# Optimization experiments

Measured on AMD Instinct MI355X. Metric: run time of the kernel, lower is better.

## Reference

```python
import jax, jax.numpy as jnp
import numpy as np

WS = 16          # window_size
OWS = 24         # overlap_win_size = int(ws*0.5) + ws
PAD = (OWS - WS) // 2
NH = 6           # num_heads


def _ln(x, g, b):
    m = jnp.mean(x, axis=-1, keepdims=True)
    v = jnp.mean((x - m) ** 2, axis=-1, keepdims=True)
    return (x - m) * jax.lax.rsqrt(v + 1e-5) * g + b


def setup_inputs() -> dict:
    key = jax.random.key(0)
    ks = jax.random.split(key, 12)
    B, H, W, C = 4, 64, 64, 180
    std = 0.02
    x = jax.random.normal(ks[0], (B, H * W, C), jnp.float32)
    y = jax.random.normal(ks[1], (B, H * W, C), jnp.float32)
    kv_w = jax.random.normal(ks[2], (2 * C, C), jnp.float32) * std
    kv_b = jnp.zeros((2 * C,), jnp.float32)
    q_w = jax.random.normal(ks[3], (C, C), jnp.float32) * std
    q_b = jnp.zeros((C,), jnp.float32)
    rpb = jax.random.normal(ks[4], ((WS + OWS - 1) ** 2, NH), jnp.float32) * std
    proj_w = jax.random.normal(ks[5], (C, C), jnp.float32) * std
    proj_b = jnp.zeros((C,), jnp.float32)
    fc1_w = jax.random.normal(ks[6], (4 * C, C), jnp.float32) * std
    fc1_b = jnp.zeros((4 * C,), jnp.float32)
    fc2_w = jax.random.normal(ks[7], (C, 4 * C), jnp.float32) * std
    fc2_b = jnp.zeros((C,), jnp.float32)
    norm1_g = jnp.ones((C,), jnp.float32); norm1_b = jnp.zeros((C,), jnp.float32)
    norm2_g = jnp.ones((C,), jnp.float32); norm2_b = jnp.zeros((C,), jnp.float32)
    # relative position index (HAT-style OCA): query coords vs extended window coords
    co = np.stack(np.meshgrid(np.arange(WS), np.arange(WS), indexing='ij')).reshape(2, -1)   # 2, ws*ws
    ce = np.stack(np.meshgrid(np.arange(OWS), np.arange(OWS), indexing='ij')).reshape(2, -1) # 2, ows*ows
    rel = (ce[:, None, :] - co[:, :, None]).transpose(1, 2, 0) + (WS - 1)  # nq, n, 2 in [0, ws+ows-2]
    rpi = jnp.asarray(rel[..., 0] * (WS + OWS - 1) + rel[..., 1], jnp.int32)  # [256, 576]
    return {
        'x': x, 'y': y,
        'norm1_g': norm1_g, 'norm1_b': norm1_b,
        'kv_w': kv_w, 'kv_b': kv_b, 'q_w': q_w, 'q_b': q_b,
        'rpb': rpb, 'proj_w': proj_w, 'proj_b': proj_b,
        'norm2_g': norm2_g, 'norm2_b': norm2_b,
        'fc1_w': fc1_w, 'fc1_b': fc1_b, 'fc2_w': fc2_w, 'fc2_b': fc2_b,
        'rpi': rpi, 'h': 64, 'w': 64,
    }


def reference(x, y, norm1_g, norm1_b, kv_w, kv_b, q_w, q_b, rpb, proj_w, proj_b,
              norm2_g, norm2_b, fc1_w, fc1_b, fc2_w, fc2_b, rpi, h, w):
    b, L, c = x.shape
    nh = NH
    d = c // nh
    scale = d ** -0.5
    nwh, nww = h // WS, w // WS
    nq, n = WS * WS, OWS * OWS

    shortcut = x
    xn = _ln(x, norm1_g, norm1_b).reshape(b, h, w, c)
    yn = _ln(y, norm1_g, norm1_b).reshape(b, h, w, c)

    kv = xn @ kv_w.T + kv_b                                  # b,h,w,2c
    q = yn @ q_w.T + q_b                                     # b,h,w,c

    # kv -> [2, b, c, h, w] then pad spatially and extract overlapping windows (nn.Unfold)
    kv = kv.reshape(b, h, w, 2, c).transpose(3, 0, 4, 1, 2)  # 2,b,c,h,w
    kvp = jnp.pad(kv, ((0, 0), (0, 0), (0, 0), (PAD, PAD), (PAD, PAD)))
    hh = jnp.arange(nwh)[:, None] * WS + jnp.arange(OWS)[None, :]   # [nwh, OWS]
    ww = jnp.arange(nww)[:, None] * WS + jnp.arange(OWS)[None, :]   # [nww, OWS]
    patches = kvp[:, :, :, hh][:, :, :, :, :, ww]            # 2,b,c,nwh,OWS,nww,OWS
    kvw = patches.transpose(0, 1, 3, 5, 4, 6, 2).reshape(2, b * nwh * nww, n, c)
    kwin, vwin = kvw[0], kvw[1]                              # [b_, n, c]

    # non-overlapping query windows (window_partition)
    qwin = q.reshape(b, nwh, WS, nww, WS, c).transpose(0, 1, 3, 2, 4, 5).reshape(-1, nq, c)
    b_ = qwin.shape[0]

    qh = qwin.reshape(b_, nq, nh, d).transpose(0, 2, 1, 3) * scale
    kh = kwin.reshape(b_, n, nh, d).transpose(0, 2, 1, 3)
    vh = vwin.reshape(b_, n, nh, d).transpose(0, 2, 1, 3)

    attn = jnp.einsum('bhqd,bhkd->bhqk', qh, kh)             # [b_, nh, nq, n]
    bias = rpb[rpi.reshape(-1)].reshape(nq, n, nh).transpose(2, 0, 1)  # [nh, nq, n]
    attn = jax.nn.softmax(attn + bias[None], axis=-1)
    out = jnp.einsum('bhqk,bhkd->bhqd', attn, vh).transpose(0, 2, 1, 3).reshape(b_, nq, c)

    # window_reverse
    out = out.reshape(b, nwh, nww, WS, WS, c).transpose(0, 1, 3, 2, 4, 5).reshape(b, h * w, c)

    xo = out @ proj_w.T + proj_b + shortcut
    xn2 = _ln(xo, norm2_g, norm2_b)
    mlp = jax.nn.gelu(xn2 @ fc1_w.T + fc1_b, approximate=False) @ fc2_w.T + fc2_b
    return xo + mlp
```

## Files before the change

### kernel.cpp

```cpp
#include <hip/hip_runtime.h>

typedef __bf16 bf16;
typedef __bf16 bf16x8 __attribute__((ext_vector_type(8)));
typedef __bf16 bf16x4 __attribute__((ext_vector_type(4)));
typedef __bf16 bf16x2 __attribute__((ext_vector_type(2)));
typedef float f32x4 __attribute__((ext_vector_type(4)));

static __device__ __forceinline__ bf16x8 ld8(const bf16* p) {
    return *reinterpret_cast<const bf16x8*>(p);
}
static __device__ __forceinline__ bf16x4 ld4(const bf16* p) {
    return *reinterpret_cast<const bf16x4*>(p);
}
static __device__ __forceinline__ bf16x8 ld8_b32(const bf16* p) {
    bf16x8 v;
#pragma unroll
    for (int i = 0; i < 4; ++i) {
        bf16x2 t = *reinterpret_cast<const bf16x2*>(p + i * 2);
        v[i * 2] = t[0]; v[i * 2 + 1] = t[1];
    }
    return v;
}
static __device__ __forceinline__ bf16x8 zero8() {
    bf16x8 v;
#pragma unroll
    for (int i = 0; i < 8; ++i) v[i] = (bf16)0.f;
    return v;
}

#define MFMA16(a, b, c) __builtin_amdgcn_mfma_f32_16x16x32_bf16((a), (b), (c), 0, 0, 0)

template <int BK, int KPAD>
static __device__ __forceinline__ void stage_tile(const bf16* __restrict__ g,
                                                  bf16* __restrict__ lds, int tid) {
    constexpr int CPR = BK / 8;
    constexpr int NP = 64 * CPR / 256;
#pragma unroll
    for (int p = 0; p < NP; ++p) {
        int idx = p * 256 + tid;
        int row = idx / CPR, cg = idx % CPR;
        bf16x8 v = ld8(g + (long)row * KPAD + cg * 8);
        *reinterpret_cast<bf16x8*>(lds + row * 200 + cg * 8) = v;
    }
}

__global__ __launch_bounds__(256) void prep_kernel(
    const float* __restrict__ kv_w, const float* __restrict__ q_w,
    const float* __restrict__ proj_w, const float* __restrict__ fc1_w,
    const float* __restrict__ fc2_w, const float* __restrict__ rpb,
    const int* __restrict__ rpi,
    bf16* __restrict__ wkv, bf16* __restrict__ wq, bf16* __restrict__ wproj,
    bf16* __restrict__ wfc1, bf16* __restrict__ wfc2, bf16* __restrict__ biast)
{
    int i = blockIdx.x * 256 + threadIdx.x;
    if (i < 73728) {
        int n = i / 192, k = i % 192;
        float v = (n < 360 && k < 180) ? kv_w[n * 180 + k] : 0.f;
        wkv[i] = (bf16)v;
    } else if (i < 122880) {
        int j = i - 73728; int n = j / 192, k = j % 192;
        float v = (n < 180 && k < 180) ? q_w[n * 180 + k] : 0.f;
        wq[j] = (bf16)v;
    } else if (i < 172032) {
        int j = i - 122880; int n = j / 192, k = j % 192;
        int hh = k >> 5, d = k & 31;
        float v = (n < 180 && d < 30) ? proj_w[n * 180 + hh * 30 + d] : 0.f;
        wproj[j] = (bf16)v;
    } else if (i < 319488) {
        int j = i - 172032; int n = j / 192, k = j % 192;
        float v = (n < 720 && k < 180) ? fc1_w[n * 180 + k] : 0.f;
        wfc1[j] = (bf16)v;
    } else if (i < 507904) {
        int j = i - 319488; int n = j / 736, k = j % 736;
        float v = (n < 180 && k < 720) ? fc2_w[n * 720 + k] : 0.f;
        wfc2[j] = (bf16)v;
    } else if (i < 1392640) {
        int t = i - 507904;
        int h = t / 147456, rem = t % 147456;
        int q = rem / 576, key = rem % 576;
        biast[t] = (bf16)rpb[rpi[q * 576 + key] * 6 + h];
    }
}

__global__ __launch_bounds__(256) void ln_kernel(
    const float* __restrict__ srcA, const float* __restrict__ srcB,
    const float* __restrict__ g, const float* __restrict__ b,
    bf16* __restrict__ dst)
{
    int wave = threadIdx.x >> 6, lane = threadIdx.x & 63;
    int row = blockIdx.x * 4 + wave;
    const float* sp = (row < 16384) ? (srcA + row * 180) : (srcB + (row - 16384) * 180);
    float v0 = sp[lane];
    float v1 = sp[lane + 64];
    float v2 = (lane < 52) ? sp[lane + 128] : 0.f;
    float s = v0 + v1 + v2;
    float sq = v0 * v0 + v1 * v1 + v2 * v2;
#pragma unroll
    for (int m = 32; m >= 1; m >>= 1) {
        s += __shfl_xor(s, m);
        sq += __shfl_xor(sq, m);
    }
    float mean = s * (1.f / 180.f);
    float var = sq * (1.f / 180.f) - mean * mean;
    float rs = rsqrtf(var + 1e-5f);
    bf16* dp = dst + (long)row * 192;
    dp[lane] = (bf16)((v0 - mean) * rs * g[lane] + b[lane]);
    dp[lane + 64] = (bf16)((v1 - mean) * rs * g[lane + 64] + b[lane + 64]);
    float o2 = (lane < 52) ? ((v2 - mean) * rs * g[lane + 128] + b[lane + 128]) : 0.f;
    dp[lane + 128] = (bf16)o2;
}

__global__ __launch_bounds__(256, 3) void gemm_kvq(
    const bf16* __restrict__ xn, const bf16* __restrict__ yn,
    const bf16* __restrict__ wkv, const bf16* __restrict__ wq,
    const float* __restrict__ kv_b, const float* __restrict__ q_b,
    bf16* __restrict__ kvbuf, bf16* __restrict__ qbuf)
{
    const int tid = threadIdx.x, wave = tid >> 6, lane = tid & 63;
    const int llo = lane & 15, quad = lane >> 4;
    const int ng = blockIdx.y;
    const bool isq = ng >= 6;
    const bf16* A = isq ? yn : xn;
    const bf16* W = isq ? (wq + (ng - 6) * 64 * 192) : (wkv + ng * 64 * 192);
    const int tm = blockIdx.x * 64;

    __shared__ __align__(16) bf16 Sa[64 * 200];
    __shared__ __align__(16) bf16 Sb[64 * 200];
    stage_tile<192, 192>(A + (long)tm * 192, Sa, tid);
    stage_tile<192, 192>(W, Sb, tid);
    __syncthreads();

    f32x4 acc[4];
#pragma unroll
    for (int nt = 0; nt < 4; ++nt)
#pragma unroll
        for (int r = 0; r < 4; ++r) acc[nt][r] = 0.f;

#pragma unroll
    for (int kt = 0; kt < 6; ++kt) {
        bf16x8 a = ld8(Sa + (wave * 16 + llo) * 200 + kt * 32 + quad * 8);
#pragma unroll
        for (int nt = 0; nt < 4; ++nt) {
            bf16x8 b = ld8(Sb + (nt * 16 + llo) * 200 + kt * 32 + quad * 8);
            acc[nt] = MFMA16(a, b, acc[nt]);
        }
    }

#pragma unroll
    for (int nt = 0; nt < 4; ++nt)
#pragma unroll
        for (int r = 0; r < 4; ++r) {
            int m = tm + wave * 16 + quad * 4 + r;
            int n = ng * 64 + nt * 16 + llo;
            if (!isq) {
                if (n < 360) {
                    float v = acc[nt][r] + kv_b[n];
                    int nn = n % 180;
                    int col = (n / 180) * 192 + (nn / 30) * 32 + (nn % 30);
                    kvbuf[(long)m * 384 + col] = (bf16)v;
                }
            } else {
                int nq = n - 384;
                if (nq < 180) {
                    float v = (acc[nt][r] + q_b[nq]) * 0.18257418583505537f;
                    int col = (nq / 30) * 32 + (nq % 30);
                    qbuf[(long)m * 192 + col] = (bf16)v;
                }
            }
        }
}

__global__ __launch_bounds__(512, 6) void attn_kernel(
    const bf16* __restrict__ qbuf, const bf16* __restrict__ kvbuf,
    const bf16* __restrict__ biast, bf16* __restrict__ obuf)
{
    const int qhalf = blockIdx.x & 1;
    const int head = (blockIdx.x >> 1) % 6;
    const int win = blockIdx.x / 12;
    const int bb = win / 16, wi = (win % 16) / 4, wj = win % 4;
    const int tid = threadIdx.x;
    const int wave = tid >> 6, lane = tid & 63;
    const int llo = lane & 15, quad = lane >> 4;
    const int qbase = qhalf * 128 + wave * 16;

    __shared__ bf16 Kc[64][40];
    __shared__ bf16 Vt[32][74];
    __shared__ bf16 Ps[8][16][72];

    const int u = tid & 255;
    const int tloc = u >> 2, dq = u & 3;
    const bool isV = tid >= 256;
    int aa = tloc / 24, w0 = tloc % 24;

    const int q0 = qbase + llo;
    const int gr_q = bb * 4096 + (wi * 16 + (q0 >> 4)) * 64 + (wj * 16 + (q0 & 15));
    const bf16x8 qf = ld8(qbuf + (long)gr_q * 192 + head * 32 + quad * 8);

    bf16x8 stage = zero8();
    {
        int gy = wi * 16 + aa - 4, gx = wj * 16 + w0 - 4;
        if ((unsigned)gy < 64u && (unsigned)gx < 64u) {
            long gr = (long)(bb * 4096 + gy * 64 + gx) * 384;
            stage = ld8(kvbuf + gr + (isV ? 192 : 0) + head * 32 + dq * 8);
        }
    }

    f32x4 o[2];
    float m_run = -1e30f, l_run = 0.f;
#pragma unroll
    for (int n2 = 0; n2 < 2; ++n2)
#pragma unroll
        for (int r = 0; r < 4; ++r) o[n2][r] = 0.f;

    for (int c = 0; c < 9; ++c) {
        const int kb = c * 64;
        __syncthreads();
        if (!isV) {
            *reinterpret_cast<bf16x8*>(&Kc[tloc][dq * 8]) = stage;
        } else {
#pragma unroll
            for (int j = 0; j < 8; ++j) Vt[dq * 8 + j][tloc] = stage[j];
        }
        __syncthreads();

        if (c < 8) {
            w0 += 16; aa += 2;
            if (w0 >= 24) { w0 -= 24; ++aa; }
            int gy = wi * 16 + aa - 4, gx = wj * 16 + w0 - 4;
            stage = zero8();
            if ((unsigned)gy < 64u && (unsigned)gx < 64u) {
                long gr = (long)(bb * 4096 + gy * 64 + gx) * 384;
                stage = ld8(kvbuf + gr + (isV ? 192 : 0) + head * 32 + dq * 8);
            }
        }

        f32x4 s[4];
#pragma unroll
        for (int kt = 0; kt < 4; ++kt) {
            bf16x8 kf = ld8(&Kc[kt * 16 + llo][quad * 8]);
            f32x4 zc;
            zc[0] = 0.f; zc[1] = 0.f; zc[2] = 0.f; zc[3] = 0.f;
            s[kt] = MFMA16(kf, qf, zc);
        }

#pragma unroll
        for (int kt = 0; kt < 4; ++kt) {
            bf16x4 bv = ld4(biast + ((long)head * 256 + q0) * 576 + kb + kt * 16 + quad * 4);
#pragma unroll
            for (int r = 0; r < 4; ++r) s[kt][r] += (float)bv[r];
        }

        float mx = s[0][0];
#pragma unroll
        for (int kt = 0; kt < 4; ++kt)
#pragma unroll
            for (int r = 0; r < 4; ++r) mx = fmaxf(mx, s[kt][r]);
        mx = fmaxf(mx, __shfl_xor(mx, 16));
        mx = fmaxf(mx, __shfl_xor(mx, 32));
        float m_new = fmaxf(m_run, mx);
        float alpha = __expf(m_run - m_new);
        float ls = 0.f;
#pragma unroll
        for (int kt = 0; kt < 4; ++kt)
#pragma unroll
            for (int r = 0; r < 4; ++r) {
                float p = __expf(s[kt][r] - m_new);
                s[kt][r] = p;
                ls += p;
            }
        ls += __shfl_xor(ls, 16);
        ls += __shfl_xor(ls, 32);
        l_run = l_run * alpha + ls;
        m_run = m_new;

#pragma unroll
        for (int r = 0; r < 4; ++r) {
            float a = __shfl(alpha, quad * 4 + r);
            o[0][r] *= a;
            o[1][r] *= a;
        }

#pragma unroll
        for (int kt = 0; kt < 4; ++kt) {
            bf16x4 pv;
#pragma unroll
            for (int r = 0; r < 4; ++r) pv[r] = (bf16)s[kt][r];
            *reinterpret_cast<bf16x4*>(&Ps[wave][llo][kt * 16 + quad * 4]) = pv;
        }

#pragma unroll
        for (int kt2 = 0; kt2 < 2; ++kt2) {
            bf16x8 pa = ld8(&Ps[wave][llo][kt2 * 32 + quad * 8]);
#pragma unroll
            for (int n2 = 0; n2 < 2; ++n2) {
                bf16x8 vb = ld8_b32(&Vt[n2 * 16 + llo][kt2 * 32 + quad * 8]);
                o[n2] = MFMA16(pa, vb, o[n2]);
            }
        }
    }

    float linv = 1.f / l_run;
#pragma unroll
    for (int r = 0; r < 4; ++r) {
        float li = __shfl(linv, quad * 4 + r);
        int q = qbase + quad * 4 + r;
        int gr = bb * 4096 + (wi * 16 + (q >> 4)) * 64 + (wj * 16 + (q & 15));
#pragma unroll
        for (int n2 = 0; n2 < 2; ++n2)
            obuf[(long)gr * 192 + head * 32 + n2 * 16 + llo] = (bf16)(o[n2][r] * li);
    }
}

__global__ __launch_bounds__(256, 3) void gemm_projln(
    const bf16* __restrict__ obuf, const bf16* __restrict__ wproj,
    const float* __restrict__ proj_b, const float* __restrict__ x,
    const float* __restrict__ g, const float* __restrict__ bln,
    float* __restrict__ xo, bf16* __restrict__ xn2)
{
    const int tid = threadIdx.x, wave = tid >> 6, lane = tid & 63;
    const int llo = lane & 15, quad = lane >> 4;
    const int mbase = blockIdx.x * 64;

    __shared__ __align__(16) bf16 Sa[64 * 200];
    __shared__ __align__(16) bf16 Sb[64 * 200];
    stage_tile<192, 192>(obuf + (long)mbase * 192, Sa, tid);

    f32x4 acc[12];
#pragma unroll
    for (int nt = 0; nt < 12; ++nt)
#pragma unroll
        for (int r = 0; r < 4; ++r) acc[nt][r] = 0.f;

    for (int nc = 0; nc < 3; ++nc) {
        if (nc) __syncthreads();
        stage_tile<192, 192>(wproj + (long)nc * 64 * 192, Sb, tid);
        __syncthreads();
#pragma unroll
        for (int kt = 0; kt < 6; ++kt) {
            bf16x8 a = ld8(Sa + (wave * 16 + llo) * 200 + kt * 32 + quad * 8);
#pragma unroll
            for (int nt = 0; nt < 4; ++nt) {
                bf16x8 b = ld8(Sb + (nt * 16 + llo) * 200 + kt * 32 + quad * 8);
                acc[nc * 4 + nt] = MFMA16(a, b, acc[nc * 4 + nt]);
            }
        }
    }

#pragma unroll
    for (int r = 0; r < 4; ++r) {
        int m = mbase + wave * 16 + quad * 4 + r;
        float v[12];
        float sum = 0.f, sq = 0.f;
#pragma unroll
        for (int nt = 0; nt < 12; ++nt) {
            int n = nt * 16 + llo;
            float val = 0.f;
            if (n < 180) val = acc[nt][r] + proj_b[n] + x[(long)m * 180 + n];
            v[nt] = val;
            sum += val; sq += val * val;
        }
#pragma unroll
        for (int msk = 1; msk <= 8; msk <<= 1) {
            sum += __shfl_xor(sum, msk);
            sq  += __shfl_xor(sq, msk);
        }
        float mean = sum * (1.f / 180.f);
        float var = sq * (1.f / 180.f) - mean * mean;
        float rs = rsqrtf(var + 1e-5f);
#pragma unroll
        for (int nt = 0; nt < 12; ++nt) {
            int n = nt * 16 + llo;
            if (n < 180) {
                xo[(long)m * 180 + n] = v[nt];
                xn2[(long)m * 192 + n] = (bf16)((v[nt] - mean) * rs * g[n] + bln[n]);
            } else {
                xn2[(long)m * 192 + n] = (bf16)0.f;
            }
        }
    }
}

template <int KPAD, int NREAL, int OSTRIDE, int MODE>
__global__ __launch_bounds__(256, 3) void gemm_ep(
    const bf16* __restrict__ A, const bf16* __restrict__ W,
    const float* __restrict__ bias, const float* __restrict__ resid,
    void* __restrict__ outp)
{
    const int tid = threadIdx.x, wave = tid >> 6, lane = tid & 63;
    const int llo = lane & 15, quad = lane >> 4;
    const int tm = blockIdx.x * 64;
    const int tn = blockIdx.y * 64;

    __shared__ __align__(16) bf16 Sa[64 * 200];
    __shared__ __align__(16) bf16 Sb[64 * 200];

    f32x4 acc[4];
#pragma unroll
    for (int nt = 0; nt < 4; ++nt)
#pragma unroll
        for (int r = 0; r < 4; ++r) acc[nt][r] = 0.f;

    constexpr int NCH = (KPAD + 191) / 192;
#pragma unroll
    for (int c = 0; c < NCH; ++c) {
        const int koff = c * 192;
        const bool full = (koff + 192 <= KPAD);
        if (c) __syncthreads();
        if (full) {
            stage_tile<192, KPAD>(A + (long)tm * KPAD + koff, Sa, tid);
            stage_tile<192, KPAD>(W + (long)tn * KPAD + koff, Sb, tid);
        } else {
            stage_tile<160, KPAD>(A + (long)tm * KPAD + koff, Sa, tid);
            stage_tile<160, KPAD>(W + (long)tn * KPAD + koff, Sb, tid);
        }
        __syncthreads();
        const int nkt = full ? 6 : 5;
        for (int kt = 0; kt < nkt; ++kt) {
            bf16x8 a = ld8(Sa + (wave * 16 + llo) * 200 + kt * 32 + quad * 8);
#pragma unroll
            for (int nt = 0; nt < 4; ++nt) {
                bf16x8 b = ld8(Sb + (nt * 16 + llo) * 200 + kt * 32 + quad * 8);
                acc[nt] = MFMA16(a, b, acc[nt]);
            }
        }
    }

#pragma unroll
    for (int nt = 0; nt < 4; ++nt)
#pragma unroll
        for (int r = 0; r < 4; ++r) {
            int m = tm + wave * 16 + quad * 4 + r;
            int n = tn + nt * 16 + llo;
            if (n >= NREAL) continue;
            float v = acc[nt][r] + bias[n];
            if (MODE == 2) {
                ((float*)outp)[(long)m * OSTRIDE + n] = v + resid[(long)m * 180 + n];
            } else {
                float gel = 0.5f * v * (1.f + erff(v * 0.7071067811865475f));
                ((bf16*)outp)[(long)m * OSTRIDE + n] = (bf16)gel;
            }
        }
}

extern "C" void kernel_launch(void* const* d_in, const int* in_sizes, int n_in,
                              void* d_out, int out_size, void* d_ws, size_t ws_size,
                              hipStream_t stream) {
    const float* x      = (const float*)d_in[0];
    const float* y      = (const float*)d_in[1];
    const float* n1g    = (const float*)d_in[2];
    const float* n1b    = (const float*)d_in[3];
    const float* kv_w   = (const float*)d_in[4];
    const float* kv_b   = (const float*)d_in[5];
    const float* q_w    = (const float*)d_in[6];
    const float* q_b    = (const float*)d_in[7];
    const float* rpb    = (const float*)d_in[8];
    const float* proj_w = (const float*)d_in[9];
    const float* proj_b = (const float*)d_in[10];
    const float* n2g    = (const float*)d_in[11];
    const float* n2b    = (const float*)d_in[12];
    const float* fc1_w  = (const float*)d_in[13];
    const float* fc1_b  = (const float*)d_in[14];
    const float* fc2_w  = (const float*)d_in[15];
    const float* fc2_b  = (const float*)d_in[16];
    const int*   rpi    = (const int*)d_in[17];

    char* ws = (char*)d_ws;
    bf16* xn    = (bf16*)(ws + 0);
    bf16* yn    = (bf16*)(ws + 6291456);
    bf16* qbuf  = (bf16*)(ws + 12582912);
    bf16* kvbuf = (bf16*)(ws + 18874368);
    bf16* obuf  = (bf16*)(ws + 31457280);
    float* xo   = (float*)(ws + 37748736);
    bf16* biast = (bf16*)(ws + 49545216);
    bf16* wkv   = (bf16*)(ws + 51314688);
    bf16* wq    = (bf16*)(ws + 51462144);
    bf16* wproj = (bf16*)(ws + 51560448);
    bf16* wfc1  = (bf16*)(ws + 51658752);
    bf16* wfc2  = (bf16*)(ws + 51953664);
    bf16* hmid  = (bf16*)(ws + 6291456);
    bf16* xn2   = xn;

    prep_kernel<<<5440, 256, 0, stream>>>(kv_w, q_w, proj_w, fc1_w, fc2_w, rpb, rpi,
                                          wkv, wq, wproj, wfc1, wfc2, biast);
    ln_kernel<<<8192, 256, 0, stream>>>(x, y, n1g, n1b, xn);
    gemm_kvq<<<dim3(256, 9), 256, 0, stream>>>(xn, yn, wkv, wq, kv_b, q_b, kvbuf, qbuf);
    attn_kernel<<<768, 512, 0, stream>>>(qbuf, kvbuf, biast, obuf);
    gemm_projln<<<256, 256, 0, stream>>>(obuf, wproj, proj_b, x, n2g, n2b, xo, xn2);
    gemm_ep<192, 720, 736, 3><<<dim3(256, 12), 256, 0, stream>>>(xn2, wfc1, fc1_b, nullptr, hmid);
    gemm_ep<736, 180, 180, 2><<<dim3(256, 3), 256, 0, stream>>>(hmid, wfc2, fc2_b, xo, (float*)d_out);
}
```

Baseline: 221.5 us.

## Register-prefetch weight tiles, double-buffer attention K/V, reorder bias layout

The kvq and fc1 GEMM blocks now keep the A tile resident in LDS and loop over three N tiles each, with the next weight tile prefetched into registers during compute. The grids shrink accordingly. The fc2 GEMM and proj GEMM prefetch their next K chunk into registers in the same way. The attention kernel double-buffers its K/V LDS tiles so one barrier per chunk is removed. The relative-position bias is re-laid out in prep so each lane reads contiguous 4-element groups matching the MFMA fragment order. These changes target global-load latency and barrier stalls, at the cost of more registers per thread and fewer blocks in flight for the GEMMs.

```diff
diff --git a/kernel.cpp b/kernel.cpp
--- a/kernel.cpp
+++ b/kernel.cpp
@@ -41,6 +41,30 @@
         int row = idx / CPR, cg = idx % CPR;
         bf16x8 v = ld8(g + (long)row * KPAD + cg * 8);
         *reinterpret_cast<bf16x8*>(lds + row * 200 + cg * 8) = v;
+    }
+}
+template <int BK, int KPAD>
+static __device__ __forceinline__ void load_chunk(const bf16* __restrict__ g,
+                                                  bf16x8* r, int tid) {
+    constexpr int CPR = BK / 8;
+    constexpr int NP = 64 * CPR / 256;
+#pragma unroll
+    for (int p = 0; p < NP; ++p) {
+        int idx = p * 256 + tid;
+        int row = idx / CPR, cg = idx % CPR;
+        r[p] = ld8(g + (long)row * KPAD + cg * 8);
+    }
+}
+template <int BK>
+static __device__ __forceinline__ void store_chunk(bf16* __restrict__ lds,
+                                                   const bf16x8* r, int tid) {
+    constexpr int CPR = BK / 8;
+    constexpr int NP = 64 * CPR / 256;
+#pragma unroll
+    for (int p = 0; p < NP; ++p) {
+        int idx = p * 256 + tid;
+        int row = idx / CPR, cg = idx % CPR;
+        *reinterpret_cast<bf16x8*>(lds + row * 200 + cg * 8) = r[p];
     }
 }
 
@@ -76,8 +100,15 @@
         wfc2[j] = (bf16)v;
     } else if (i < 1392640) {
         int t = i - 507904;
-        int h = t / 147456, rem = t % 147456;
-        int q = rem / 576, key = rem % 576;
+        int r = t & 3;
+        int lane = (t >> 2) & 63;
+        int tmp2 = t >> 8;
+        int kg = tmp2 % 36;
+        int tmp3 = tmp2 / 36;
+        int qg = tmp3 & 15;
+        int h = tmp3 >> 4;
+        int q = qg * 16 + (lane & 15);
+        int key = kg * 16 + ((lane >> 4) << 2) + r;
         biast[t] = (bf16)rpb[rpi[q * 576 + key] * 6 + h];
     }
 }
@@ -110,7 +141,7 @@
     dp[lane + 128] = (bf16)o2;
 }
 
-__global__ __launch_bounds__(256, 3) void gemm_kvq(
+__global__ __launch_bounds__(256, 4) void gemm_kvq(
     const bf16* __restrict__ xn, const bf16* __restrict__ yn,
     const bf16* __restrict__ wkv, const bf16* __restrict__ wq,
     const float* __restrict__ kv_b, const float* __restrict__ q_b,
@@ -118,61 +149,71 @@
 {
     const int tid = threadIdx.x, wave = tid >> 6, lane = tid & 63;
     const int llo = lane & 15, quad = lane >> 4;
-    const int ng = blockIdx.y;
-    const bool isq = ng >= 6;
+    const int bz = blockIdx.y;
+    const bool isq = (bz == 2);
     const bf16* A = isq ? yn : xn;
-    const bf16* W = isq ? (wq + (ng - 6) * 64 * 192) : (wkv + ng * 64 * 192);
+    const bf16* Wbase = isq ? wq : (wkv + (long)bz * 3 * 64 * 192);
     const int tm = blockIdx.x * 64;
 
     __shared__ __align__(16) bf16 Sa[64 * 200];
     __shared__ __align__(16) bf16 Sb[64 * 200];
+
     stage_tile<192, 192>(A + (long)tm * 192, Sa, tid);
-    stage_tile<192, 192>(W, Sb, tid);
-    __syncthreads();
-
-    f32x4 acc[4];
-#pragma unroll
-    for (int nt = 0; nt < 4; ++nt)
-#pragma unroll
-        for (int r = 0; r < 4; ++r) acc[nt][r] = 0.f;
-
-#pragma unroll
-    for (int kt = 0; kt < 6; ++kt) {
-        bf16x8 a = ld8(Sa + (wave * 16 + llo) * 200 + kt * 32 + quad * 8);
-#pragma unroll
-        for (int nt = 0; nt < 4; ++nt) {
-            bf16x8 b = ld8(Sb + (nt * 16 + llo) * 200 + kt * 32 + quad * 8);
-            acc[nt] = MFMA16(a, b, acc[nt]);
-        }
-    }
-
-#pragma unroll
-    for (int nt = 0; nt < 4; ++nt)
-#pragma unroll
-        for (int r = 0; r < 4; ++r) {
-            int m = tm + wave * 16 + quad * 4 + r;
-            int n = ng * 64 + nt * 16 + llo;
-            if (!isq) {
-                if (n < 360) {
-                    float v = acc[nt][r] + kv_b[n];
-                    int nn = n % 180;
-                    int col = (n / 180) * 192 + (nn / 30) * 32 + (nn % 30);
-                    kvbuf[(long)m * 384 + col] = (bf16)v;
+    bf16x8 wreg[6];
+    load_chunk<192, 192>(Wbase, wreg, tid);
+
+    for (int s = 0; s < 3; ++s) {
+        if (s) __syncthreads();
+        store_chunk<192>(Sb, wreg, tid);
+        __syncthreads();
+        if (s < 2) load_chunk<192, 192>(Wbase + (long)(s + 1) * 64 * 192, wreg, tid);
+
+        f32x4 acc[4];
+#pragma unroll
+        for (int nt = 0; nt < 4; ++nt)
+#pragma unroll
+            for (int r = 0; r < 4; ++r) acc[nt][r] = 0.f;
+#pragma unroll
+        for (int kt = 0; kt < 6; ++kt) {
+            bf16x8 a = ld8(Sa + (wave * 16 + llo) * 200 + kt * 32 + quad * 8);
+#pragma unroll
+            for (int nt = 0; nt < 4; ++nt) {
+                bf16x8 b = ld8(Sb + (nt * 16 + llo) * 200 + kt * 32 + quad * 8);
+                acc[nt] = MFMA16(a, b, acc[nt]);
+            }
+        }
+
+        const int g = bz * 3 + s;
+#pragma unroll
+        for (int nt = 0; nt < 4; ++nt)
+#pragma unroll
+            for (int r = 0; r < 4; ++r) {
+                int m = tm + wave * 16 + quad * 4 + r;
+                int n = g * 64 + nt * 16 + llo;
+                if (!isq) {
+                    if (n < 360) {
+                        float v = acc[nt][r] + kv_b[n];
+                        int nn = n % 180;
+                        int col = (n / 180) * 192 + (nn / 30) * 32 + (nn % 30);
+                        kvbuf[(long)m * 384 + col] = (bf16)v;
+                    }
+                } else {
+                    int nq = n - 384;
+                    if (nq < 180) {
+                        float v = (acc[nt][r] + q_b[nq]) * 0.18257418583505537f;
+                        int col = (nq / 30) * 32 + (nq % 30);
+                        qbuf[(long)m * 192 + col] = (bf16)v;
+                    }
                 }
-            } else {
-                int nq = n - 384;
-                if (nq < 180) {
-                    float v = (acc[nt][r] + q_b[nq]) * 0.18257418583505537f;
-                    int col = (nq / 30) * 32 + (nq % 30);
-                    qbuf[(long)m * 192 + col] = (bf16)v;
-                }
-            }
-        }
+            }
+    }
 }
 
 __global__ __launch_bounds__(512, 6) void attn_kernel(
-    const bf16* __restrict__ qbuf, const bf16* __restrict__ kvbuf,
-    const bf16* __restrict__ biast, bf16* __restrict__ obuf)
+    const bf16* __restrict__ qbuf,
+    const bf16* __restrict__ kvbuf,
+    const bf16* __restrict__ biast,
+    bf16* __restrict__ obuf)
 {
     const int qhalf = blockIdx.x & 1;
     const int head = (blockIdx.x >> 1) % 6;
@@ -182,9 +223,10 @@
     const int wave = tid >> 6, lane = tid & 63;
     const int llo = lane & 15, quad = lane >> 4;
     const int qbase = qhalf * 128 + wave * 16;
-
-    __shared__ bf16 Kc[64][40];
-    __shared__ bf16 Vt[32][74];
+    const int qg = qhalf * 8 + wave;
+
+    __shared__ bf16 Kc[2][64][40];
+    __shared__ bf16 Vt[2][32][74];
     __shared__ bf16 Ps[8][16][72];
 
     const int u = tid & 255;
@@ -195,15 +237,23 @@
     const int q0 = qbase + llo;
     const int gr_q = bb * 4096 + (wi * 16 + (q0 >> 4)) * 64 + (wj * 16 + (q0 & 15));
     const bf16x8 qf = ld8(qbuf + (long)gr_q * 192 + head * 32 + quad * 8);
-
-    bf16x8 stage = zero8();
+    const bf16* bbase = biast + ((long)(head * 16 + qg) * 36) * 256 + lane * 4;
+
     {
         int gy = wi * 16 + aa - 4, gx = wj * 16 + w0 - 4;
+        bf16x8 st = zero8();
         if ((unsigned)gy < 64u && (unsigned)gx < 64u) {
             long gr = (long)(bb * 4096 + gy * 64 + gx) * 384;
-            stage = ld8(kvbuf + gr + (isV ? 192 : 0) + head * 32 + dq * 8);
-        }
-    }
+            st = ld8(kvbuf + gr + (isV ? 192 : 0) + head * 32 + dq * 8);
+        }
+        if (!isV) {
+            *reinterpret_cast<bf16x8*>(&Kc[0][tloc][dq * 8]) = st;
+        } else {
+#pragma unroll
+            for (int j = 0; j < 8; ++j) Vt[0][dq * 8 + j][tloc] = st[j];
+        }
+    }
+    __syncthreads();
 
     f32x4 o[2];
     float m_run = -1e30f, l_run = 0.f;
@@ -213,16 +263,9 @@
         for (int r = 0; r < 4; ++r) o[n2][r] = 0.f;
 
     for (int c = 0; c < 9; ++c) {
-        const int kb = c * 64;
-        __syncthreads();
-        if (!isV) {
-            *reinterpret_cast<bf16x8*>(&Kc[tloc][dq * 8]) = stage;
-        } else {
-#pragma unroll
-            for (int j = 0; j < 8; ++j) Vt[dq * 8 + j][tloc] = stage[j];
-        }
-        __syncthreads();
-
+        const int cur = c & 1;
+
+        bf16x8 stage;
         if (c < 8) {
             w0 += 16; aa += 2;
             if (w0 >= 24) { w0 -= 24; ++aa; }
@@ -237,7 +280,7 @@
         f32x4 s[4];
 #pragma unroll
         for (int kt = 0; kt < 4; ++kt) {
-            bf16x8 kf = ld8(&Kc[kt * 16 + llo][quad * 8]);
+            bf16x8 kf = ld8(&Kc[cur][kt * 16 + llo][quad * 8]);
             f32x4 zc;
             zc[0] = 0.f; zc[1] = 0.f; zc[2] = 0.f; zc[3] = 0.f;
             s[kt] = MFMA16(kf, qf, zc);
@@ -245,7 +288,7 @@
 
 #pragma unroll
         for (int kt = 0; kt < 4; ++kt) {
-            bf16x4 bv = ld4(biast + ((long)head * 256 + q0) * 576 + kb + kt * 16 + quad * 4);
+            bf16x4 bv = ld4(bbase + (c * 4 + kt) * 256);
 #pragma unroll
             for (int r = 0; r < 4; ++r) s[kt][r] += (float)bv[r];
         }
@@ -293,9 +336,19 @@
             bf16x8 pa = ld8(&Ps[wave][llo][kt2 * 32 + quad * 8]);
 #pragma unroll
             for (int n2 = 0; n2 < 2; ++n2) {
-                bf16x8 vb = ld8_b32(&Vt[n2 * 16 + llo][kt2 * 32 + quad * 8]);
+                bf16x8 vb = ld8_b32(&Vt[cur][n2 * 16 + llo][kt2 * 32 + quad * 8]);
                 o[n2] = MFMA16(pa, vb, o[n2]);
             }
+        }
+
+        if (c < 8) {
+            if (!isV) {
+                *reinterpret_cast<bf16x8*>(&Kc[1 - cur][tloc][dq * 8]) = stage;
+            } else {
+#pragma unroll
+                for (int j = 0; j < 8; ++j) Vt[1 - cur][dq * 8 + j][tloc] = stage[j];
+            }
+            __syncthreads();
         }
     }
 
@@ -324,6 +377,8 @@
     __shared__ __align__(16) bf16 Sa[64 * 200];
     __shared__ __align__(16) bf16 Sb[64 * 200];
     stage_tile<192, 192>(obuf + (long)mbase * 192, Sa, tid);
+    bf16x8 wreg[6];
+    load_chunk<192, 192>(wproj, wreg, tid);
 
     f32x4 acc[12];
 #pragma unroll
@@ -333,8 +388,9 @@
 
     for (int nc = 0; nc < 3; ++nc) {
         if (nc) __syncthreads();
-        stage_tile<192, 192>(wproj + (long)nc * 64 * 192, Sb, tid);
+        store_chunk<192>(Sb, wreg, tid);
         __syncthreads();
+        if (nc < 2) load_chunk<192, 192>(wproj + (long)(nc + 1) * 64 * 192, wreg, tid);
 #pragma unroll
         for (int kt = 0; kt < 6; ++kt) {
             bf16x8 a = ld8(Sa + (wave * 16 + llo) * 200 + kt * 32 + quad * 8);
@@ -380,11 +436,62 @@
     }
 }
 
-template <int KPAD, int NREAL, int OSTRIDE, int MODE>
-__global__ __launch_bounds__(256, 3) void gemm_ep(
+__global__ __launch_bounds__(256, 4) void gemm_fc1(
+    const bf16* __restrict__ A, const bf16* __restrict__ W,
+    const float* __restrict__ bias, bf16* __restrict__ outp)
+{
+    const int tid = threadIdx.x, wave = tid >> 6, lane = tid & 63;
+    const int llo = lane & 15, quad = lane >> 4;
+    const int tm = blockIdx.x * 64;
+    const int bz = blockIdx.y;
+    const bf16* Wbase = W + (long)bz * 3 * 64 * 192;
+
+    __shared__ __align__(16) bf16 Sa[64 * 200];
+    __shared__ __align__(16) bf16 Sb[64 * 200];
+    stage_tile<192, 192>(A + (long)tm * 192, Sa, tid);
+    bf16x8 wreg[6];
+    load_chunk<192, 192>(Wbase, wreg, tid);
+
+    for (int s = 0; s < 3; ++s) {
+        if (s) __syncthreads();
+        store_chunk<192>(Sb, wreg, tid);
+        __syncthreads();
+        if (s < 2) load_chunk<192, 192>(Wbase + (long)(s + 1) * 64 * 192, wreg, tid);
+
+        f32x4 acc[4];
+#pragma unroll
+        for (int nt = 0; nt < 4; ++nt)
+#pragma unroll
+            for (int r = 0; r < 4; ++r) acc[nt][r] = 0.f;
+#pragma unroll
+        for (int kt = 0; kt < 6; ++kt) {
+            bf16x8 a = ld8(Sa + (wave * 16 + llo) * 200 + kt * 32 + quad * 8);
+#pragma unroll
+            for (int nt = 0; nt < 4; ++nt) {
+                bf16x8 b = ld8(Sb + (nt * 16 + llo) * 200 + kt * 32 + quad * 8);
+                acc[nt] = MFMA16(a, b, acc[nt]);
+            }
+        }
+
+        const int nb = (bz * 3 + s) * 64;
+#pragma unroll
+        for (int nt = 0; nt < 4; ++nt)
+#pragma unroll
+            for (int r = 0; r < 4; ++r) {
+                int m = tm + wave * 16 + quad * 4 + r;
+                int n = nb + nt * 16 + llo;
+                if (n >= 720) continue;
+                float v = acc[nt][r] + bias[n];
+                float gel = 0.5f * v * (1.f + erff(v * 0.7071067811865475f));
+                outp[(long)m * 736 + n] = (bf16)gel;
+            }
+    }
+}
+
+__global__ __launch_bounds__(256, 4) void gemm_fc2(
     const bf16* __restrict__ A, const bf16* __restrict__ W,
     const float* __restrict__ bias, const float* __restrict__ resid,
-    void* __restrict__ outp)
+    float* __restrict__ outp)
 {
     const int tid = threadIdx.x, wave = tid >> 6, lane = tid & 63;
     const int llo = lane & 15, quad = lane >> 4;
@@ -394,27 +501,33 @@
     __shared__ __align__(16) bf16 Sa[64 * 200];
     __shared__ __align__(16) bf16 Sb[64 * 200];
 
+    const bf16* Ap = A + (long)tm * 736;
+    const bf16* Wp = W + (long)tn * 736;
+
+    bf16x8 ar[6], wr[6];
+    load_chunk<192, 736>(Ap, ar, tid);
+    load_chunk<192, 736>(Wp, wr, tid);
+
     f32x4 acc[4];
 #pragma unroll
     for (int nt = 0; nt < 4; ++nt)
 #pragma unroll
         for (int r = 0; r < 4; ++r) acc[nt][r] = 0.f;
 
-    constexpr int NCH = (KPAD + 191) / 192;
-#pragma unroll
-    for (int c = 0; c < NCH; ++c) {
-        const int koff = c * 192;
-        const bool full = (koff + 192 <= KPAD);
+#pragma unroll
+    for (int c = 0; c < 4; ++c) {
         if (c) __syncthreads();
-        if (full) {
-            stage_tile<192, KPAD>(A + (long)tm * KPAD + koff, Sa, tid);
-            stage_tile<192, KPAD>(W + (long)tn * KPAD + koff, Sb, tid);
-        } else {
-            stage_tile<160, KPAD>(A + (long)tm * KPAD + koff, Sa, tid);
-            stage_tile<160, KPAD>(W + (long)tn * KPAD + koff, Sb, tid);
-        }
+        if (c < 3) { store_chunk<192>(Sa, ar, tid); store_chunk<192>(Sb, wr, tid); }
+        else       { store_chunk<160>(Sa, ar, tid); store_chunk<160>(Sb, wr, tid); }
         __syncthreads();
-        const int nkt = full ? 6 : 5;
+        if (c < 2) {
+            load_chunk<192, 736>(Ap + (c + 1) * 192, ar, tid);
+            load_chunk<192, 736>(Wp + (c + 1) * 192, wr, tid);
+        } else if (c == 2) {
+            load_chunk<160, 736>(Ap + 576, ar, tid);
+            load_chunk<160, 736>(Wp + 576, wr, tid);
+        }
+        const int nkt = (c == 3) ? 5 : 6;
         for (int kt = 0; kt < nkt; ++kt) {
             bf16x8 a = ld8(Sa + (wave * 16 + llo) * 200 + kt * 32 + quad * 8);
 #pragma unroll
@@ -431,14 +544,9 @@
         for (int r = 0; r < 4; ++r) {
             int m = tm + wave * 16 + quad * 4 + r;
             int n = tn + nt * 16 + llo;
-            if (n >= NREAL) continue;
+            if (n >= 180) continue;
             float v = acc[nt][r] + bias[n];
-            if (MODE == 2) {
-                ((float*)outp)[(long)m * OSTRIDE + n] = v + resid[(long)m * 180 + n];
-            } else {
-                float gel = 0.5f * v * (1.f + erff(v * 0.7071067811865475f));
-                ((bf16*)outp)[(long)m * OSTRIDE + n] = (bf16)gel;
-            }
+            outp[(long)m * 180 + n] = v + resid[(long)m * 180 + n];
         }
 }
 
@@ -483,9 +591,9 @@
     prep_kernel<<<5440, 256, 0, stream>>>(kv_w, q_w, proj_w, fc1_w, fc2_w, rpb, rpi,
                                           wkv, wq, wproj, wfc1, wfc2, biast);
     ln_kernel<<<8192, 256, 0, stream>>>(x, y, n1g, n1b, xn);
-    gemm_kvq<<<dim3(256, 9), 256, 0, stream>>>(xn, yn, wkv, wq, kv_b, q_b, kvbuf, qbuf);
+    gemm_kvq<<<dim3(256, 3), 256, 0, stream>>>(xn, yn, wkv, wq, kv_b, q_b, kvbuf, qbuf);
     attn_kernel<<<768, 512, 0, stream>>>(qbuf, kvbuf, biast, obuf);
     gemm_projln<<<256, 256, 0, stream>>>(obuf, wproj, proj_b, x, n2g, n2b, xo, xn2);
-    gemm_ep<192, 720, 736, 3><<<dim3(256, 12), 256, 0, stream>>>(xn2, wfc1, fc1_b, nullptr, hmid);
-    gemm_ep<736, 180, 180, 2><<<dim3(256, 3), 256, 0, stream>>>(hmid, wfc2, fc2_b, xo, (float*)d_out);
-}
+    gemm_fc1<<<dim3(256, 4), 256, 0, stream>>>(xn2, wfc1, fc1_b, hmid);
+    gemm_fc2<<<dim3(256, 3), 256, 0, stream>>>(hmid, wfc2, fc2_b, xo, (float*)d_out);
+}
```

Measured after the change: 211.9 us. 4.4% less time.
